# Kernel optimization log

Hardware: AMD Instinct MI355X
Metric: run time of the kernel (lower is better)

## Reference

```python
import jax, jax.numpy as jnp
import numpy as np

B, T, I, H, L, O = 128, 1024, 256, 1024, 2, 128


def setup_inputs() -> dict:
    key = jax.random.key(0)
    ks = jax.random.split(key, 11)
    s = 0.02  # small init scale for stable gates
    inp = {
        "x": jax.random.normal(ks[0], (B, T, I), dtype=jnp.float32),
        # PyTorch LSTM params, gate order (i, f, g, o) stacked along 4H
        "w_ih0": jax.random.normal(ks[1], (4 * H, I), dtype=jnp.float32) * s,
        "w_hh0": jax.random.normal(ks[2], (4 * H, H), dtype=jnp.float32) * s,
        "b_ih0": jax.random.normal(ks[3], (4 * H,), dtype=jnp.float32) * s,
        "b_hh0": jax.random.normal(ks[4], (4 * H,), dtype=jnp.float32) * s,
        "w_ih1": jax.random.normal(ks[5], (4 * H, H), dtype=jnp.float32) * s,
        "w_hh1": jax.random.normal(ks[6], (4 * H, H), dtype=jnp.float32) * s,
        "b_ih1": jax.random.normal(ks[7], (4 * H,), dtype=jnp.float32) * s,
        "b_hh1": jax.random.normal(ks[8], (4 * H,), dtype=jnp.float32) * s,
        "w_out": jax.random.normal(ks[9], (O, H), dtype=jnp.float32) * s,
        "b_out": jax.random.normal(ks[10], (O,), dtype=jnp.float32) * s,
    }
    return inp


def _lstm_layer(x, w_ih, w_hh, b_ih, b_hh):
    # x: [B, T, Din] -> ys: [B, T, H], h_T: [B, H]
    # Precompute input-side gate projections for all timesteps (one big GEMM).
    xg = jnp.einsum("bti,gi->btg", x, w_ih) + b_ih + b_hh  # [B, T, 4H]
    h0 = jnp.zeros((x.shape[0], H), dtype=x.dtype)
    c0 = jnp.zeros((x.shape[0], H), dtype=x.dtype)

    def step(carry, xg_t):
        h, c = carry
        gates = xg_t + h @ w_hh.T  # [B, 4H]
        i, f, g, o = jnp.split(gates, 4, axis=-1)
        i = jax.nn.sigmoid(i)
        f = jax.nn.sigmoid(f)
        g = jnp.tanh(g)
        o = jax.nn.sigmoid(o)
        c_new = f * c + i * g
        h_new = o * jnp.tanh(c_new)
        return (h_new, c_new), h_new

    (h_T, _), ys = jax.lax.scan(step, (h0, c0), jnp.swapaxes(xg, 0, 1))
    return jnp.swapaxes(ys, 0, 1), h_T


def reference(x, w_ih0, w_hh0, b_ih0, b_hh0, w_ih1, w_hh1, b_ih1, b_hh1, w_out, b_out):
    y0, _ = _lstm_layer(x, w_ih0, w_hh0, b_ih0, b_hh0)
    _, h_last = _lstm_layer(y0, w_ih1, w_hh1, b_ih1, b_hh1)
    return h_last @ w_out.T + b_out  # [B, O]
```

## Files before the change

kernel.cpp:

```cpp
#include <hip/hip_runtime.h>
#include <hip/hip_bf16.h>

#define B_ 128
#define T_ 1024
#define I_ 256
#define H_ 1024
#define O_ 128
#define NWG 256
#define HS_ 131072

typedef __attribute__((ext_vector_type(4))) float f32x4;
typedef __attribute__((ext_vector_type(8))) short s16x8;

__device__ __forceinline__ unsigned short f2bf(float f){
  union { float f; unsigned int u; } a; a.f = f;
  unsigned int r = a.u + 0x7FFFu + ((a.u >> 16) & 1u);
  return (unsigned short)(r >> 16);
}
__device__ __forceinline__ float sigmf(float x){ return 1.f/(1.f+__expf(-x)); }
__device__ __forceinline__ float tanhf_(float x){ return 2.f/(1.f+__expf(-2.f*x)) - 1.f; }

__device__ __forceinline__ void ld_frag(s16x8 &d, const unsigned short* p){
  asm volatile("global_load_dwordx4 %0, %1, off sc1" : "=v"(d) : "v"(p) : "memory");
}
__device__ __forceinline__ void ld_f4c(f32x4 &d, const float* p){
  asm volatile("global_load_dwordx4 %0, %1, off sc1" : "=v"(d) : "v"(p) : "memory");
}
__device__ __forceinline__ void st_h(unsigned short* p, unsigned short v){
  __hip_atomic_store(p, v, __ATOMIC_RELAXED, __HIP_MEMORY_SCOPE_AGENT);
}
__device__ __forceinline__ void st_f(float* p, float v){
  __hip_atomic_store(p, v, __ATOMIC_RELAXED, __HIP_MEMORY_SCOPE_AGENT);
}

template<int N>
__device__ __forceinline__ void waitpair(s16x8 &x, s16x8 &y){
  if      constexpr (N==14) asm volatile("s_waitcnt vmcnt(14)" : "+v"(x), "+v"(y) :: "memory");
  else if constexpr (N==12) asm volatile("s_waitcnt vmcnt(12)" : "+v"(x), "+v"(y) :: "memory");
  else if constexpr (N==10) asm volatile("s_waitcnt vmcnt(10)" : "+v"(x), "+v"(y) :: "memory");
  else if constexpr (N==8)  asm volatile("s_waitcnt vmcnt(8)"  : "+v"(x), "+v"(y) :: "memory");
  else if constexpr (N==6)  asm volatile("s_waitcnt vmcnt(6)"  : "+v"(x), "+v"(y) :: "memory");
  else if constexpr (N==4)  asm volatile("s_waitcnt vmcnt(4)"  : "+v"(x), "+v"(y) :: "memory");
  else if constexpr (N==2)  asm volatile("s_waitcnt vmcnt(2)"  : "+v"(x), "+v"(y) :: "memory");
  else                      asm volatile("s_waitcnt vmcnt(0)"  : "+v"(x), "+v"(y) :: "memory");
}
__device__ __forceinline__ void vm_drain(){
  asm volatile("s_waitcnt vmcnt(0)" ::: "memory");
}

__device__ __forceinline__ void bar_arrive(unsigned* base, int gwg, int tid){
  vm_drain();
  __syncthreads();
  if (tid == 0)
    __hip_atomic_fetch_add(&base[(gwg & 7) << 6], 1u, __ATOMIC_RELAXED, __HIP_MEMORY_SCOPE_AGENT);
}
__device__ __forceinline__ void bar_wait(unsigned* base, unsigned tgt32, int tid){
  if (tid < 8){
    while (__hip_atomic_load(&base[tid << 6], __ATOMIC_RELAXED, __HIP_MEMORY_SCOPE_AGENT) < tgt32)
      __builtin_amdgcn_s_sleep(2);
  }
  __syncthreads();
}


__global__ void k_cast_x(const float* __restrict__ x, unsigned short* __restrict__ xb, int n4){
  int i = blockIdx.x*blockDim.x + threadIdx.x;
  if (i >= n4) return;
  f32x4 v = reinterpret_cast<const f32x4*>(x)[i];
  ushort4 o;
  o.x = f2bf(v[0]); o.y = f2bf(v[1]); o.z = f2bf(v[2]); o.w = f2bf(v[3]);
  reinterpret_cast<ushort4*>(xb)[i] = o;
}

__global__ void k_prep_w0(const float* __restrict__ wih, const float* __restrict__ whh,
                          unsigned short* __restrict__ out){
  int n = blockIdx.x*256 + threadIdx.x;
  int j = n & 7, r = (n >> 3) & 15;
  int t = n >> 7;
  int kb = t % 160, gw = t / 160;
  int k = kb*8 + j;
  int grow = (r >> 2)*H_ + gw*4 + (r & 3);
  float v = (k < I_) ? wih[grow*I_ + k] : whh[grow*H_ + (k - I_)];
  out[n] = f2bf(v);
}

__global__ void k_prep_w1(const float* __restrict__ wih, const float* __restrict__ whh,
                          unsigned short* __restrict__ out){
  int n = blockIdx.x*256 + threadIdx.x;
  int j = n & 7, r = (n >> 3) & 15;
  int t = n >> 7;
  int kb = t & 255, gw = t >> 8;
  int k = kb*8 + j;
  int grow = (r >> 2)*H_ + gw*4 + (r & 3);
  float v = (k < H_) ? wih[grow*H_ + k] : whh[grow*H_ + (k - H_)];
  out[n] = f2bf(v);
}

__global__ void k_prep_b(const float* __restrict__ bi0, const float* __restrict__ bh0,
                         const float* __restrict__ bi1, const float* __restrict__ bh1,
                         float* __restrict__ b0, float* __restrict__ b1){
  int n = blockIdx.x*256 + threadIdx.x;
  int layer = n >> 12; int rem = n & 4095;
  int gw = rem >> 4, r = rem & 15;
  int grow = (r >> 2)*H_ + gw*4 + (r & 3);
  if (layer == 0) b0[rem] = bi0[grow] + bh0[grow];
  else            b1[rem] = bi1[grow] + bh1[grow];
}


struct KArgs {
  const unsigned short* xb;
  const float* x32;
  const unsigned short* w0l;
  const unsigned short* w1l;
  const float* b0l;
  const float* b1l;
  unsigned short* h0;
  unsigned short* h1;
  float* hfin;
  const float* wout;
  const float* bout;
  float* y;
  unsigned* cnt;
};

__device__ __forceinline__ void epi(f32x4 (&acc)[2], float (&cs)[2][4], float bias,
                                    unsigned short* __restrict__ hw,
                                    float* __restrict__ hfin,
                                    int wv, int lane, int gwg){
  const int u  = lane & 3;
  const int g0 = (lane >> 2) & 3;
  const int bq = lane >> 4;
  const int ug = (gwg << 2) + u;
  const int kc = ug >> 5;
  const int kg = (ug >> 3) & 3;
  const int jj = ug & 7;
  #pragma unroll
  for (int btl = 0; btl < 2; ++btl){
    const int rb = wv*2 + btl;
    #pragma unroll
    for (int r = 0; r < 4; ++r){
      float pre = acc[btl][r] + bias;
      float q1 = __shfl_xor(pre, 4);
      float q2 = __shfl_xor(pre, 8);
      float q3 = __shfl_xor(pre, 12);
      float iv = (g0==0)?pre:((g0==1)?q1:((g0==2)?q2:q3));
      float fv = (g0==1)?pre:((g0==0)?q1:((g0==3)?q2:q3));
      float gv = (g0==2)?pre:((g0==3)?q1:((g0==0)?q2:q3));
      float ov = (g0==3)?pre:((g0==2)?q1:((g0==1)?q2:q3));
      iv = sigmf(iv); fv = sigmf(fv); gv = tanhf_(gv); ov = sigmf(ov);
      float cn = fv*cs[btl][r] + iv*gv;
      cs[btl][r] = cn;
      float h = ov*tanhf_(cn);
      if (g0 == 0){
        int brow = bq*4 + r;
        int eidx = (((rb*32 + kc) << 9) + (kg*16 + brow)*8 + jj);
        st_h(&hw[eidx], f2bf(h));
        if (hfin) st_f(&hfin[(rb*16 + brow)*H_ + ug], h);
      }
    }
  }
}

#define STEP0(i, NW) { \
  const int s_ = (i) & 7; \
  s16x8 wfn_ = wfc; \
  if ((i) + 1 < 32) wfn_ = *(const s16x8*)(sW0 + ((9 + (i)) << 9) + (lane << 3)); \
  waitpair<NW>(fr[s_][0], fr[s_][1]); \
  acc0[0] = __builtin_amdgcn_mfma_f32_16x16x32_bf16(fr[s_][0], wfc, acc0[0], 0, 0, 0); \
  acc0[1] = __builtin_amdgcn_mfma_f32_16x16x32_bf16(fr[s_][1], wfc, acc0[1], 0, 0, 0); \
  if ((i) + 8 < 32){ \
    ld_frag(fr[s_][0], h0r + ((rdA + (i) + 8) << 9) + l8); \
    ld_frag(fr[s_][1], h0r + ((rdB + (i) + 8) << 9) + l8); } \
  wfc = wfn_; }

#define STEP1(i, NW) { \
  const int s_ = (i) & 7; \
  s16x8 wfn_ = wfc; \
  if ((i) + 1 < 64) wfn_ = *(const s16x8*)(sW1 + (((i) + 1) << 9) + (lane << 3)); \
  waitpair<NW>(fr[s_][0], fr[s_][1]); \
  acc1[0] = __builtin_amdgcn_mfma_f32_16x16x32_bf16(fr[s_][0], wfc, acc1[0], 0, 0, 0); \
  acc1[1] = __builtin_amdgcn_mfma_f32_16x16x32_bf16(fr[s_][1], wfc, acc1[1], 0, 0, 0); \
  if ((i) + 8 < 64){ const int j_ = (i) + 8; \
    const unsigned short* b_ = (j_ < 32) ? h0r : h1r; \
    ld_frag(fr[s_][0], b_ + ((rdA + (j_ & 31)) << 9) + l8); \
    ld_frag(fr[s_][1], b_ + ((rdB + (j_ & 31)) << 9) + l8); } \
  wfc = wfn_; }

__global__ void __launch_bounds__(256, 1) k_lstm(KArgs a){
  extern __shared__ char smem[];
  unsigned short* sW0 = (unsigned short*)smem;
  unsigned short* sW1 = (unsigned short*)(smem + 40960);
  float* sB    = (float*)(smem + 106496);

  const int tid  = threadIdx.x;
  const int gwg  = blockIdx.x;
  const int wv   = tid >> 6;
  const int lane = tid & 63;
  const int lrow = lane & 15;
  const int kgrp = lane >> 4;
  const int koff = kgrp << 3;

  {
    const s16x8* s0 = (const s16x8*)a.w0l + gwg*2560;
    s16x8* d0 = (s16x8*)sW0;
    for (int i = tid; i < 2560; i += 256) d0[i] = s0[i];
    const s16x8* s1 = (const s16x8*)a.w1l + gwg*4096;
    s16x8* d1 = (s16x8*)sW1;
    for (int i = tid; i < 4096; i += 256) d1[i] = s1[i];
    if (tid < 16){ sB[tid] = a.b0l[gwg*16 + tid]; sB[16 + tid] = a.b1l[gwg*16 + tid]; }
  }
  __syncthreads();

  const float bias0 = sB[lrow];
  const float bias1 = sB[16 + lrow];
  float c0s[2][4] = {{0,0,0,0},{0,0,0,0}};
  float c1s[2][4] = {{0,0,0,0},{0,0,0,0}};

  const int rdA = (wv*2 + 0) << 5;
  const int rdB = (wv*2 + 1) << 5;
  const int l8  = lane << 3;
  const size_t xoff0 = (size_t)((wv*2 + 0)*16 + lrow)*(T_*I_) + koff;
  const size_t xoff1 = (size_t)((wv*2 + 1)*16 + lrow)*(T_*I_) + koff;
  const f32x4 z = {0.f, 0.f, 0.f, 0.f};

  int m3 = 0, m3p1 = 1, m3p2 = 2;

  for (int p = 0; p <= T_; ++p){
    const unsigned short* __restrict__ h0r = a.h0 + m3p2*HS_;
    const unsigned short* __restrict__ h1r = a.h1 + m3p1*HS_;
    unsigned short* __restrict__ h0w = a.h0 + m3  *HS_;
    unsigned short* __restrict__ h1w = a.h1 + m3p2*HS_;

    f32x4 acc0[2] = {z, z};
    if (p < T_){
      if (a.xb){
        const unsigned short* xp0 = a.xb + xoff0 + p*I_;
        const unsigned short* xp1 = a.xb + xoff1 + p*I_;
        #pragma unroll
        for (int kc = 0; kc < 8; ++kc){
          s16x8 wf = *(const s16x8*)(sW0 + (kc << 9) + (lane << 3));
          s16x8 a0 = *(const s16x8*)(xp0 + (kc << 5));
          s16x8 a1 = *(const s16x8*)(xp1 + (kc << 5));
          acc0[0] = __builtin_amdgcn_mfma_f32_16x16x32_bf16(a0, wf, acc0[0], 0, 0, 0);
          acc0[1] = __builtin_amdgcn_mfma_f32_16x16x32_bf16(a1, wf, acc0[1], 0, 0, 0);
        }
      } else {
        const float* fx0 = a.x32 + xoff0 + p*I_;
        const float* fx1 = a.x32 + xoff1 + p*I_;
        #pragma unroll
        for (int kc = 0; kc < 8; ++kc){
          s16x8 wf = *(const s16x8*)(sW0 + (kc << 9) + (lane << 3));
          union { s16x8 v; unsigned short us[8]; } t0, t1;
          f32x4 p00 = *(const f32x4*)(fx0 + (kc << 5));
          f32x4 p01 = *(const f32x4*)(fx0 + (kc << 5) + 4);
          f32x4 p10 = *(const f32x4*)(fx1 + (kc << 5));
          f32x4 p11 = *(const f32x4*)(fx1 + (kc << 5) + 4);
          #pragma unroll
          for (int j2 = 0; j2 < 4; ++j2){
            t0.us[j2] = f2bf(p00[j2]); t0.us[4+j2] = f2bf(p01[j2]);
            t1.us[j2] = f2bf(p10[j2]); t1.us[4+j2] = f2bf(p11[j2]);
          }
          acc0[0] = __builtin_amdgcn_mfma_f32_16x16x32_bf16(t0.v, wf, acc0[0], 0, 0, 0);
          acc0[1] = __builtin_amdgcn_mfma_f32_16x16x32_bf16(t1.v, wf, acc0[1], 0, 0, 0);
        }
      }
    }

    if (p > 0) bar_wait(a.cnt, 32u * (unsigned)p, tid);

    if (p < T_){
      vm_drain();
      s16x8 fr[8][2];
      #pragma unroll
      for (int s2 = 0; s2 < 8; ++s2){
        ld_frag(fr[s2][0], h0r + ((rdA + s2) << 9) + l8);
        ld_frag(fr[s2][1], h0r + ((rdB + s2) << 9) + l8);
      }
      s16x8 wfc = *(const s16x8*)(sW0 + (8 << 9) + (lane << 3));
      #pragma unroll
      for (int i = 0; i < 25; ++i) STEP0(i, 14);
      STEP0(25,12); STEP0(26,10); STEP0(27,8); STEP0(28,6);
      STEP0(29,4);  STEP0(30,2);  STEP0(31,0);
      epi(acc0, c0s, bias0, h0w, nullptr, wv, lane, gwg);
    }

    if (p > 0){
      f32x4 acc1[2] = {z, z};
      vm_drain();
      s16x8 fr[8][2];
      #pragma unroll
      for (int s2 = 0; s2 < 8; ++s2){
        ld_frag(fr[s2][0], h0r + ((rdA + s2) << 9) + l8);
        ld_frag(fr[s2][1], h0r + ((rdB + s2) << 9) + l8);
      }
      s16x8 wfc = *(const s16x8*)(sW1 + (lane << 3));
      #pragma unroll
      for (int i = 0; i < 57; ++i) STEP1(i, 14);
      STEP1(57,12); STEP1(58,10); STEP1(59,8); STEP1(60,6);
      STEP1(61,4);  STEP1(62,2);  STEP1(63,0);
      epi(acc1, c1s, bias1, h1w, (p == T_) ? a.hfin : nullptr, wv, lane, gwg);
    }

    bar_arrive(a.cnt, gwg, tid);

    m3 = m3p1; m3p1 = m3p2; m3p2 = (m3p2 == 2) ? 0 : m3p2 + 1;
  }

  bar_wait(a.cnt, 32u * (unsigned)(T_ + 1), tid);

  if (gwg < 64){
    const int b = (gwg >> 3)*16 + (tid >> 4);
    const int o = (gwg & 7)*16 + (tid & 15);
    const float* hb = a.hfin + b*H_;
    const f32x4* wr = (const f32x4*)(a.wout + o*H_);
    float s = a.bout[o];
    for (int g = 0; g < 32; ++g){
      f32x4 t0,t1,t2,t3,t4,t5,t6,t7;
      ld_f4c(t0, hb + g*32 +  0); ld_f4c(t1, hb + g*32 +  4);
      ld_f4c(t2, hb + g*32 +  8); ld_f4c(t3, hb + g*32 + 12);
      ld_f4c(t4, hb + g*32 + 16); ld_f4c(t5, hb + g*32 + 20);
      ld_f4c(t6, hb + g*32 + 24); ld_f4c(t7, hb + g*32 + 28);
      asm volatile("s_waitcnt vmcnt(0)"
        : "+v"(t0),"+v"(t1),"+v"(t2),"+v"(t3),"+v"(t4),"+v"(t5),"+v"(t6),"+v"(t7) :: "memory");
      const f32x4 w0 = wr[g*8+0], w1 = wr[g*8+1], w2 = wr[g*8+2], w3 = wr[g*8+3];
      const f32x4 w4 = wr[g*8+4], w5 = wr[g*8+5], w6 = wr[g*8+6], w7 = wr[g*8+7];
      s += t0[0]*w0[0]+t0[1]*w0[1]+t0[2]*w0[2]+t0[3]*w0[3];
      s += t1[0]*w1[0]+t1[1]*w1[1]+t1[2]*w1[2]+t1[3]*w1[3];
      s += t2[0]*w2[0]+t2[1]*w2[1]+t2[2]*w2[2]+t2[3]*w2[3];
      s += t3[0]*w3[0]+t3[1]*w3[1]+t3[2]*w3[2]+t3[3]*w3[3];
      s += t4[0]*w4[0]+t4[1]*w4[1]+t4[2]*w4[2]+t4[3]*w4[3];
      s += t5[0]*w5[0]+t5[1]*w5[1]+t5[2]*w5[2]+t5[3]*w5[3];
      s += t6[0]*w6[0]+t6[1]*w6[1]+t6[2]*w6[2]+t6[3]*w6[3];
      s += t7[0]*w7[0]+t7[1]*w7[1]+t7[2]*w7[2]+t7[3]*w7[3];
    }
    a.y[b*O_ + o] = s;
  }
}


extern "C" void kernel_launch(void* const* d_in, const int* in_sizes, int n_in,
                              void* d_out, int out_size, void* d_ws, size_t ws_size,
                              hipStream_t stream){
  const float* x    = (const float*)d_in[0];
  const float* wih0 = (const float*)d_in[1];
  const float* whh0 = (const float*)d_in[2];
  const float* bih0 = (const float*)d_in[3];
  const float* bhh0 = (const float*)d_in[4];
  const float* wih1 = (const float*)d_in[5];
  const float* whh1 = (const float*)d_in[6];
  const float* bih1 = (const float*)d_in[7];
  const float* bhh1 = (const float*)d_in[8];
  const float* wout = (const float*)d_in[9];
  const float* bout = (const float*)d_in[10];
  float* y = (float*)d_out;

  char* ws = (char*)d_ws;
  size_t off = 0;
  auto alloc = [&](size_t n){ char* p = ws + off; off += (n + 255) & ~(size_t)255; return p; };

  unsigned* cnt = (unsigned*)alloc(2048);
  unsigned short* w0l = (unsigned short*)alloc((size_t)256*160*16*8*2);
  unsigned short* w1l = (unsigned short*)alloc((size_t)256*256*16*8*2);
  float* b0l  = (float*)alloc(256*16*4);
  float* b1l  = (float*)alloc(256*16*4);
  unsigned short* h0 = (unsigned short*)alloc((size_t)3*HS_*2);
  unsigned short* h1 = (unsigned short*)alloc((size_t)3*HS_*2);
  float* hfin = (float*)alloc((size_t)B_*H_*4);
  unsigned short* xb = nullptr;
  size_t xb_bytes = (size_t)B_*T_*I_*2;
  if (ws_size >= off + xb_bytes + 256) xb = (unsigned short*)alloc(xb_bytes);

  hipMemsetAsync(cnt, 0, 2048, stream);
  hipMemsetAsync(h0, 0, (size_t)3*HS_*2, stream);
  hipMemsetAsync(h1, 0, (size_t)3*HS_*2, stream);

  if (xb) k_cast_x<<<dim3((B_*T_*I_/4 + 255)/256), dim3(256), 0, stream>>>(x, xb, B_*T_*I_/4);
  k_prep_w0<<<dim3(5242880/256), dim3(256), 0, stream>>>(wih0, whh0, w0l);
  k_prep_w1<<<dim3(8388608/256), dim3(256), 0, stream>>>(wih1, whh1, w1l);
  k_prep_b<<<dim3(32), dim3(256), 0, stream>>>(bih0, bhh0, bih1, bhh1, b0l, b1l);

  KArgs args;
  args.xb = xb; args.x32 = x;
  args.w0l = w0l; args.w1l = w1l; args.b0l = b0l; args.b1l = b1l;
  args.h0 = h0; args.h1 = h1; args.hfin = hfin;
  args.wout = wout; args.bout = bout; args.y = y;
  args.cnt = cnt;

  (void)hipFuncSetAttribute((const void*)k_lstm,
                            hipFuncAttributeMaxDynamicSharedMemorySize, 106624);
  void* kp[] = { (void*)&args };
  hipLaunchCooperativeKernel((void*)k_lstm, dim3(NWG), dim3(256), kp, 106624, stream);
}
```

Before: 13.86 ms.

## Share layer-0 hidden-state fragments between both LSTM layers' recurrent GEMMs

Each step previously loaded the layer-0 hidden state from global memory twice: once for layer 0's recurrent GEMM and again for the first half of layer 1's input GEMM. The loops are now fused so each loaded h0 fragment feeds both layer-0 and layer-1 MFMAs, followed by a separate loop over the layer-1 recurrent half. This cuts about a third of the per-step global fragment loads on the serial critical path. The cost is two live accumulator sets and two weight streams, which raises register pressure, plus MFMA work that is discarded at the first and last steps. A fallback to a normal launch is also added in case the cooperative launch fails.

Result: faster. 11.46 ms (median of 2 runs) (-17.3%).

```diff
diff --git a/kernel.cpp b/kernel.cpp
--- a/kernel.cpp
+++ b/kernel.cpp
@@ -162,30 +162,36 @@
   }
 }
 
-#define STEP0(i, NW) { \
+#define MFMA_(A, Bf, C) __builtin_amdgcn_mfma_f32_16x16x32_bf16(A, Bf, C, 0, 0, 0)
+
+#define FUS(i) { \
   const int s_ = (i) & 7; \
-  s16x8 wfn_ = wfc; \
-  if ((i) + 1 < 32) wfn_ = *(const s16x8*)(sW0 + ((9 + (i)) << 9) + (lane << 3)); \
+  s16x8 w0n_ = wfc, w1n_; \
+  if ((i) + 1 < 32) w0n_ = *(const s16x8*)(sW0 + ((9 + (i)) << 9) + (lane << 3)); \
+  w1n_ = *(const s16x8*)(sW1 + (((i) + 1) << 9) + (lane << 3)); \
+  waitpair<14>(fr[s_][0], fr[s_][1]); \
+  acc0[0] = MFMA_(fr[s_][0], wfc, acc0[0]); \
+  acc0[1] = MFMA_(fr[s_][1], wfc, acc0[1]); \
+  acc1[0] = MFMA_(fr[s_][0], wf1c, acc1[0]); \
+  acc1[1] = MFMA_(fr[s_][1], wf1c, acc1[1]); \
+  { const int j_ = (i) + 8; \
+    const unsigned short* b_ = (j_ < 32) ? h0r : h1r; \
+    const int c_ = j_ & 31; \
+    ld_frag(fr[s_][0], b_ + ((rdA + c_) << 9) + l8); \
+    ld_frag(fr[s_][1], b_ + ((rdB + c_) << 9) + l8); } \
+  wfc = w0n_; wf1c = w1n_; }
+
+#define ST2(j, NW) { \
+  const int s_ = (j) & 7; \
+  s16x8 w1n_ = wf1c; \
+  if ((j) + 1 < 32) w1n_ = *(const s16x8*)(sW1 + ((33 + (j)) << 9) + (lane << 3)); \
   waitpair<NW>(fr[s_][0], fr[s_][1]); \
-  acc0[0] = __builtin_amdgcn_mfma_f32_16x16x32_bf16(fr[s_][0], wfc, acc0[0], 0, 0, 0); \
-  acc0[1] = __builtin_amdgcn_mfma_f32_16x16x32_bf16(fr[s_][1], wfc, acc0[1], 0, 0, 0); \
-  if ((i) + 8 < 32){ \
-    ld_frag(fr[s_][0], h0r + ((rdA + (i) + 8) << 9) + l8); \
-    ld_frag(fr[s_][1], h0r + ((rdB + (i) + 8) << 9) + l8); } \
-  wfc = wfn_; }
-
-#define STEP1(i, NW) { \
-  const int s_ = (i) & 7; \
-  s16x8 wfn_ = wfc; \
-  if ((i) + 1 < 64) wfn_ = *(const s16x8*)(sW1 + (((i) + 1) << 9) + (lane << 3)); \
-  waitpair<NW>(fr[s_][0], fr[s_][1]); \
-  acc1[0] = __builtin_amdgcn_mfma_f32_16x16x32_bf16(fr[s_][0], wfc, acc1[0], 0, 0, 0); \
-  acc1[1] = __builtin_amdgcn_mfma_f32_16x16x32_bf16(fr[s_][1], wfc, acc1[1], 0, 0, 0); \
-  if ((i) + 8 < 64){ const int j_ = (i) + 8; \
-    const unsigned short* b_ = (j_ < 32) ? h0r : h1r; \
-    ld_frag(fr[s_][0], b_ + ((rdA + (j_ & 31)) << 9) + l8); \
-    ld_frag(fr[s_][1], b_ + ((rdB + (j_ & 31)) << 9) + l8); } \
-  wfc = wfn_; }
+  acc1[0] = MFMA_(fr[s_][0], wf1c, acc1[0]); \
+  acc1[1] = MFMA_(fr[s_][1], wf1c, acc1[1]); \
+  if ((j) + 8 < 32){ const int c_ = (j) + 8; \
+    ld_frag(fr[s_][0], h1r + ((rdA + c_) << 9) + l8); \
+    ld_frag(fr[s_][1], h1r + ((rdB + c_) << 9) + l8); } \
+  wf1c = w1n_; }
 
 __global__ void __launch_bounds__(256, 1) k_lstm(KArgs a){
   extern __shared__ char smem[];
@@ -233,6 +239,7 @@
     unsigned short* __restrict__ h1w = a.h1 + m3p2*HS_;
 
     f32x4 acc0[2] = {z, z};
+    f32x4 acc1[2] = {z, z};
     if (p < T_){
       if (a.xb){
         const unsigned short* xp0 = a.xb + xoff0 + p*I_;
@@ -242,8 +249,8 @@
           s16x8 wf = *(const s16x8*)(sW0 + (kc << 9) + (lane << 3));
           s16x8 a0 = *(const s16x8*)(xp0 + (kc << 5));
           s16x8 a1 = *(const s16x8*)(xp1 + (kc << 5));
-          acc0[0] = __builtin_amdgcn_mfma_f32_16x16x32_bf16(a0, wf, acc0[0], 0, 0, 0);
-          acc0[1] = __builtin_amdgcn_mfma_f32_16x16x32_bf16(a1, wf, acc0[1], 0, 0, 0);
+          acc0[0] = MFMA_(a0, wf, acc0[0]);
+          acc0[1] = MFMA_(a1, wf, acc0[1]);
         }
       } else {
         const float* fx0 = a.x32 + xoff0 + p*I_;
@@ -261,45 +268,32 @@
             t0.us[j2] = f2bf(p00[j2]); t0.us[4+j2] = f2bf(p01[j2]);
             t1.us[j2] = f2bf(p10[j2]); t1.us[4+j2] = f2bf(p11[j2]);
           }
-          acc0[0] = __builtin_amdgcn_mfma_f32_16x16x32_bf16(t0.v, wf, acc0[0], 0, 0, 0);
-          acc0[1] = __builtin_amdgcn_mfma_f32_16x16x32_bf16(t1.v, wf, acc0[1], 0, 0, 0);
+          acc0[0] = MFMA_(t0.v, wf, acc0[0]);
+          acc0[1] = MFMA_(t1.v, wf, acc0[1]);
         }
       }
     }
 
     if (p > 0) bar_wait(a.cnt, 32u * (unsigned)p, tid);
 
-    if (p < T_){
-      vm_drain();
+    vm_drain();
+    {
       s16x8 fr[8][2];
       #pragma unroll
       for (int s2 = 0; s2 < 8; ++s2){
         ld_frag(fr[s2][0], h0r + ((rdA + s2) << 9) + l8);
         ld_frag(fr[s2][1], h0r + ((rdB + s2) << 9) + l8);
       }
-      s16x8 wfc = *(const s16x8*)(sW0 + (8 << 9) + (lane << 3));
+      s16x8 wfc  = *(const s16x8*)(sW0 + (8 << 9) + (lane << 3));
+      s16x8 wf1c = *(const s16x8*)(sW1 + (lane << 3));
       #pragma unroll
-      for (int i = 0; i < 25; ++i) STEP0(i, 14);
-      STEP0(25,12); STEP0(26,10); STEP0(27,8); STEP0(28,6);
-      STEP0(29,4);  STEP0(30,2);  STEP0(31,0);
-      epi(acc0, c0s, bias0, h0w, nullptr, wv, lane, gwg);
-    }
-
-    if (p > 0){
-      f32x4 acc1[2] = {z, z};
-      vm_drain();
-      s16x8 fr[8][2];
+      for (int i = 0; i < 32; ++i) FUS(i);
+      if (p < T_) epi(acc0, c0s, bias0, h0w, nullptr, wv, lane, gwg);
       #pragma unroll
-      for (int s2 = 0; s2 < 8; ++s2){
-        ld_frag(fr[s2][0], h0r + ((rdA + s2) << 9) + l8);
-        ld_frag(fr[s2][1], h0r + ((rdB + s2) << 9) + l8);
-      }
-      s16x8 wfc = *(const s16x8*)(sW1 + (lane << 3));
-      #pragma unroll
-      for (int i = 0; i < 57; ++i) STEP1(i, 14);
-      STEP1(57,12); STEP1(58,10); STEP1(59,8); STEP1(60,6);
-      STEP1(61,4);  STEP1(62,2);  STEP1(63,0);
-      epi(acc1, c1s, bias1, h1w, (p == T_) ? a.hfin : nullptr, wv, lane, gwg);
+      for (int j = 0; j < 24; ++j) ST2(j, 14);
+      ST2(24,14); ST2(25,12); ST2(26,10); ST2(27,8);
+      ST2(28,6);  ST2(29,4);  ST2(30,2);  ST2(31,0);
+      if (p > 0) epi(acc1, c1s, bias1, h1w, (p == T_) ? a.hfin : nullptr, wv, lane, gwg);
     }
 
     bar_arrive(a.cnt, gwg, tid);
@@ -390,5 +384,9 @@
   (void)hipFuncSetAttribute((const void*)k_lstm,
                             hipFuncAttributeMaxDynamicSharedMemorySize, 106624);
   void* kp[] = { (void*)&args };
-  hipLaunchCooperativeKernel((void*)k_lstm, dim3(NWG), dim3(256), kp, 106624, stream);
-}
+  hipError_t e = hipLaunchCooperativeKernel((void*)k_lstm, dim3(NWG), dim3(256),
+                                            kp, 106624, stream);
+  if (e != hipSuccess){
+    k_lstm<<<dim3(NWG), dim3(256), 106624, stream>>>(args);
+  }
+}
```

## Split workgroups by layer, double per-WG tile, and use per-wave barriers with packed stores

Applied to the files above, without the earlier changes.

Workgroups are now dedicated to one layer each: 128 run layer 0 and 128 run layer 1. Each handles two hidden-unit tiles, so it issues four MFMAs per h-fragment load instead of two, halving redundant h reads per unit of work. The epilogue gathers bf16 h values with lane shuffles into 16-byte vector stores in place of scalar atomic stores. The grid barrier now arrives and waits per wave rather than per block, dropping __syncthreads from the step loop. The trade-offs are more LDS per workgroup (131 KB) and more barrier atomics per step, and the removed block-level sync could expose ordering hazards between waves.

Measured after the change: 21.06 ms. 52.0% more time.

```diff
diff --git a/kernel.cpp b/kernel.cpp
--- a/kernel.cpp
+++ b/kernel.cpp
@@ -11,6 +11,7 @@
 
 typedef __attribute__((ext_vector_type(4))) float f32x4;
 typedef __attribute__((ext_vector_type(8))) short s16x8;
+typedef __attribute__((ext_vector_type(4))) unsigned u32x4;
 
 __device__ __forceinline__ unsigned short f2bf(float f){
   union { float f; unsigned int u; } a; a.f = f;
@@ -26,8 +27,8 @@
 __device__ __forceinline__ void ld_f4c(f32x4 &d, const float* p){
   asm volatile("global_load_dwordx4 %0, %1, off sc1" : "=v"(d) : "v"(p) : "memory");
 }
-__device__ __forceinline__ void st_h(unsigned short* p, unsigned short v){
-  __hip_atomic_store(p, v, __ATOMIC_RELAXED, __HIP_MEMORY_SCOPE_AGENT);
+__device__ __forceinline__ void st16(unsigned short* p, u32x4 v){
+  asm volatile("global_store_dwordx4 %0, %1, off sc1" :: "v"(p), "v"(v) : "memory");
 }
 __device__ __forceinline__ void st_f(float* p, float v){
   __hip_atomic_store(p, v, __ATOMIC_RELAXED, __HIP_MEMORY_SCOPE_AGENT);
@@ -48,18 +49,16 @@
   asm volatile("s_waitcnt vmcnt(0)" ::: "memory");
 }
 
-__device__ __forceinline__ void bar_arrive(unsigned* base, int gwg, int tid){
+__device__ __forceinline__ void wbar_arrive(unsigned* base, int gwg, int lane){
   vm_drain();
-  __syncthreads();
-  if (tid == 0)
+  if (lane == 0)
     __hip_atomic_fetch_add(&base[(gwg & 7) << 6], 1u, __ATOMIC_RELAXED, __HIP_MEMORY_SCOPE_AGENT);
 }
-__device__ __forceinline__ void bar_wait(unsigned* base, unsigned tgt32, int tid){
-  if (tid < 8){
-    while (__hip_atomic_load(&base[tid << 6], __ATOMIC_RELAXED, __HIP_MEMORY_SCOPE_AGENT) < tgt32)
+__device__ __forceinline__ void wbar_wait(unsigned* base, unsigned tgt, int lane){
+  if (lane < 8){
+    while (__hip_atomic_load(&base[lane << 6], __ATOMIC_RELAXED, __HIP_MEMORY_SCOPE_AGENT) < tgt)
       __builtin_amdgcn_s_sleep(2);
   }
-  __syncthreads();
 }
 
 
@@ -124,77 +123,128 @@
   unsigned* cnt;
 };
 
-__device__ __forceinline__ void epi(f32x4 (&acc)[2], float (&cs)[2][4], float bias,
-                                    unsigned short* __restrict__ hw,
-                                    float* __restrict__ hfin,
-                                    int wv, int lane, int gwg){
+__device__ __forceinline__ void epiPack(f32x4 (&accL)[2], f32x4 (&accH)[2],
+                                        float (&csL)[2][4], float (&csH)[2][4],
+                                        float biasL, float biasH,
+                                        unsigned short* __restrict__ hw,
+                                        float* __restrict__ hfin,
+                                        int wv, int lane, int w){
   const int u  = lane & 3;
   const int g0 = (lane >> 2) & 3;
   const int bq = lane >> 4;
-  const int ug = (gwg << 2) + u;
-  const int kc = ug >> 5;
-  const int kg = (ug >> 3) & 3;
-  const int jj = ug & 7;
+  const int kc = w >> 2;
+  const int kg = w & 3;
   #pragma unroll
   for (int btl = 0; btl < 2; ++btl){
     const int rb = wv*2 + btl;
+    unsigned bL[4], bH[4];
     #pragma unroll
     for (int r = 0; r < 4; ++r){
-      float pre = acc[btl][r] + bias;
-      float q1 = __shfl_xor(pre, 4);
-      float q2 = __shfl_xor(pre, 8);
-      float q3 = __shfl_xor(pre, 12);
-      float iv = (g0==0)?pre:((g0==1)?q1:((g0==2)?q2:q3));
-      float fv = (g0==1)?pre:((g0==0)?q1:((g0==3)?q2:q3));
-      float gv = (g0==2)?pre:((g0==3)?q1:((g0==0)?q2:q3));
-      float ov = (g0==3)?pre:((g0==2)?q1:((g0==1)?q2:q3));
+      float preL = accL[btl][r] + biasL;
+      float q1 = __shfl_xor(preL, 4);
+      float q2 = __shfl_xor(preL, 8);
+      float q3 = __shfl_xor(preL, 12);
+      float iv = (g0==0)?preL:((g0==1)?q1:((g0==2)?q2:q3));
+      float fv = (g0==1)?preL:((g0==0)?q1:((g0==3)?q2:q3));
+      float gv = (g0==2)?preL:((g0==3)?q1:((g0==0)?q2:q3));
+      float ov = (g0==3)?preL:((g0==2)?q1:((g0==1)?q2:q3));
       iv = sigmf(iv); fv = sigmf(fv); gv = tanhf_(gv); ov = sigmf(ov);
-      float cn = fv*cs[btl][r] + iv*gv;
-      cs[btl][r] = cn;
-      float h = ov*tanhf_(cn);
-      if (g0 == 0){
+      float cnL = fv*csL[btl][r] + iv*gv;
+      csL[btl][r] = cnL;
+      float hL = ov*tanhf_(cnL);
+      float preH = accH[btl][r] + biasH;
+      q1 = __shfl_xor(preH, 4);
+      q2 = __shfl_xor(preH, 8);
+      q3 = __shfl_xor(preH, 12);
+      iv = (g0==0)?preH:((g0==1)?q1:((g0==2)?q2:q3));
+      fv = (g0==1)?preH:((g0==0)?q1:((g0==3)?q2:q3));
+      gv = (g0==2)?preH:((g0==3)?q1:((g0==0)?q2:q3));
+      ov = (g0==3)?preH:((g0==2)?q1:((g0==1)?q2:q3));
+      iv = sigmf(iv); fv = sigmf(fv); gv = tanhf_(gv); ov = sigmf(ov);
+      float cnH = fv*csH[btl][r] + iv*gv;
+      csH[btl][r] = cnH;
+      float hH = ov*tanhf_(cnH);
+      bL[r] = (unsigned)f2bf(hL);
+      bH[r] = (unsigned)f2bf(hH);
+      if (hfin && g0 == 0){
         int brow = bq*4 + r;
-        int eidx = (((rb*32 + kc) << 9) + (kg*16 + brow)*8 + jj);
-        st_h(&hw[eidx], f2bf(h));
-        if (hfin) st_f(&hfin[(rb*16 + brow)*H_ + ug], h);
+        st_f(&hfin[(rb*16 + brow)*H_ + 8*w + u], hL);
+        st_f(&hfin[(rb*16 + brow)*H_ + 8*w + 4 + u], hH);
       }
     }
-  }
-}
-
-#define STEP0(i, NW) { \
+    unsigned sh[4];
+    #pragma unroll
+    for (int r = 0; r < 4; ++r) sh[r] = (unsigned)__shfl_xor((int)bL[r^1], 1);
+    #pragma unroll
+    for (int r = 0; r < 4; ++r) bL[r] = ((u^r)&1) ? sh[r] : bL[r];
+    #pragma unroll
+    for (int r = 0; r < 4; ++r) sh[r] = (unsigned)__shfl_xor((int)bL[r^2], 2);
+    #pragma unroll
+    for (int r = 0; r < 4; ++r) bL[r] = ((u^r)&2) ? sh[r] : bL[r];
+    #pragma unroll
+    for (int r = 0; r < 4; ++r) sh[r] = (unsigned)__shfl_xor((int)bH[r^1], 1);
+    #pragma unroll
+    for (int r = 0; r < 4; ++r) bH[r] = ((u^r)&1) ? sh[r] : bH[r];
+    #pragma unroll
+    for (int r = 0; r < 4; ++r) sh[r] = (unsigned)__shfl_xor((int)bH[r^2], 2);
+    #pragma unroll
+    for (int r = 0; r < 4; ++r) bH[r] = ((u^r)&2) ? sh[r] : bH[r];
+    if (g0 == 0){
+      u32x4 val;
+      val[0] = bL[0] | (bL[1] << 16);
+      val[1] = bL[2] | (bL[3] << 16);
+      val[2] = bH[0] | (bH[1] << 16);
+      val[3] = bH[2] | (bH[3] << 16);
+      unsigned short* p = hw + (((rb*32 + kc) << 9) + (kg*16 + bq*4 + u)*8);
+      st16(p, val);
+    }
+  }
+}
+
+#define MFMA_(A, Bf, C) __builtin_amdgcn_mfma_f32_16x16x32_bf16(A, Bf, C, 0, 0, 0)
+
+#define L0S(i, NW) { \
   const int s_ = (i) & 7; \
-  s16x8 wfn_ = wfc; \
-  if ((i) + 1 < 32) wfn_ = *(const s16x8*)(sW0 + ((9 + (i)) << 9) + (lane << 3)); \
+  s16x8 wLn_ = wfLc, wHn_ = wfHc; \
+  if ((i) + 1 < 32){ \
+    wLn_ = *(const s16x8*)(sW + ((9 + (i)) << 9) + l8w); \
+    wHn_ = *(const s16x8*)(sW + 20480 + ((9 + (i)) << 9) + l8w); } \
   waitpair<NW>(fr[s_][0], fr[s_][1]); \
-  acc0[0] = __builtin_amdgcn_mfma_f32_16x16x32_bf16(fr[s_][0], wfc, acc0[0], 0, 0, 0); \
-  acc0[1] = __builtin_amdgcn_mfma_f32_16x16x32_bf16(fr[s_][1], wfc, acc0[1], 0, 0, 0); \
+  accL[0] = MFMA_(fr[s_][0], wfLc, accL[0]); \
+  accL[1] = MFMA_(fr[s_][1], wfLc, accL[1]); \
+  accH[0] = MFMA_(fr[s_][0], wfHc, accH[0]); \
+  accH[1] = MFMA_(fr[s_][1], wfHc, accH[1]); \
   if ((i) + 8 < 32){ \
     ld_frag(fr[s_][0], h0r + ((rdA + (i) + 8) << 9) + l8); \
     ld_frag(fr[s_][1], h0r + ((rdB + (i) + 8) << 9) + l8); } \
-  wfc = wfn_; }
-
-#define STEP1(i, NW) { \
+  wfLc = wLn_; wfHc = wHn_; }
+
+#define L1S(i, NW) { \
   const int s_ = (i) & 7; \
-  s16x8 wfn_ = wfc; \
-  if ((i) + 1 < 64) wfn_ = *(const s16x8*)(sW1 + (((i) + 1) << 9) + (lane << 3)); \
+  s16x8 wLn_ = wfLc, wHn_ = wfHc; \
+  if ((i) + 1 < 64){ \
+    wLn_ = *(const s16x8*)(sW + (((i) + 1) << 9) + l8w); \
+    wHn_ = *(const s16x8*)(sW + 32768 + (((i) + 1) << 9) + l8w); } \
   waitpair<NW>(fr[s_][0], fr[s_][1]); \
-  acc1[0] = __builtin_amdgcn_mfma_f32_16x16x32_bf16(fr[s_][0], wfc, acc1[0], 0, 0, 0); \
-  acc1[1] = __builtin_amdgcn_mfma_f32_16x16x32_bf16(fr[s_][1], wfc, acc1[1], 0, 0, 0); \
+  accL[0] = MFMA_(fr[s_][0], wfLc, accL[0]); \
+  accL[1] = MFMA_(fr[s_][1], wfLc, accL[1]); \
+  accH[0] = MFMA_(fr[s_][0], wfHc, accH[0]); \
+  accH[1] = MFMA_(fr[s_][1], wfHc, accH[1]); \
   if ((i) + 8 < 64){ const int j_ = (i) + 8; \
     const unsigned short* b_ = (j_ < 32) ? h0r : h1r; \
     ld_frag(fr[s_][0], b_ + ((rdA + (j_ & 31)) << 9) + l8); \
     ld_frag(fr[s_][1], b_ + ((rdB + (j_ & 31)) << 9) + l8); } \
-  wfc = wfn_; }
+  wfLc = wLn_; wfHc = wHn_; }
 
 __global__ void __launch_bounds__(256, 1) k_lstm(KArgs a){
   extern __shared__ char smem[];
-  unsigned short* sW0 = (unsigned short*)smem;
-  unsigned short* sW1 = (unsigned short*)(smem + 40960);
-  float* sB    = (float*)(smem + 106496);
+  unsigned short* sW = (unsigned short*)smem;
+  float* sB = (float*)(smem + 131072);
 
   const int tid  = threadIdx.x;
   const int gwg  = blockIdx.x;
+  const bool isL1 = gwg >= 128;
+  const int w    = gwg & 127;
   const int wv   = tid >> 6;
   const int lane = tid & 63;
   const int lrow = lane & 15;
@@ -202,24 +252,29 @@
   const int koff = kgrp << 3;
 
   {
-    const s16x8* s0 = (const s16x8*)a.w0l + gwg*2560;
-    s16x8* d0 = (s16x8*)sW0;
-    for (int i = tid; i < 2560; i += 256) d0[i] = s0[i];
-    const s16x8* s1 = (const s16x8*)a.w1l + gwg*4096;
-    s16x8* d1 = (s16x8*)sW1;
-    for (int i = tid; i < 4096; i += 256) d1[i] = s1[i];
-    if (tid < 16){ sB[tid] = a.b0l[gwg*16 + tid]; sB[16 + tid] = a.b1l[gwg*16 + tid]; }
+    if (isL1){
+      const s16x8* s1 = (const s16x8*)a.w1l + (size_t)(2*w)*4096;
+      s16x8* d = (s16x8*)sW;
+      for (int i = tid; i < 8192; i += 256) d[i] = s1[i];
+      if (tid < 32) sB[tid] = a.b1l[w*32 + tid];
+    } else {
+      const s16x8* s0 = (const s16x8*)a.w0l + (size_t)(2*w)*2560;
+      s16x8* d = (s16x8*)sW;
+      for (int i = tid; i < 5120; i += 256) d[i] = s0[i];
+      if (tid < 32) sB[tid] = a.b0l[w*32 + tid];
+    }
   }
   __syncthreads();
 
-  const float bias0 = sB[lrow];
-  const float bias1 = sB[16 + lrow];
-  float c0s[2][4] = {{0,0,0,0},{0,0,0,0}};
-  float c1s[2][4] = {{0,0,0,0},{0,0,0,0}};
+  const float biasL = sB[lrow];
+  const float biasH = sB[16 + lrow];
+  float csL[2][4] = {{0,0,0,0},{0,0,0,0}};
+  float csH[2][4] = {{0,0,0,0},{0,0,0,0}};
 
   const int rdA = (wv*2 + 0) << 5;
   const int rdB = (wv*2 + 1) << 5;
   const int l8  = lane << 3;
+  const int l8w = lane << 3;
   const size_t xoff0 = (size_t)((wv*2 + 0)*16 + lrow)*(T_*I_) + koff;
   const size_t xoff1 = (size_t)((wv*2 + 1)*16 + lrow)*(T_*I_) + koff;
   const f32x4 z = {0.f, 0.f, 0.f, 0.f};
@@ -232,82 +287,94 @@
     unsigned short* __restrict__ h0w = a.h0 + m3  *HS_;
     unsigned short* __restrict__ h1w = a.h1 + m3p2*HS_;
 
-    f32x4 acc0[2] = {z, z};
-    if (p < T_){
+    f32x4 accL[2] = {z, z};
+    f32x4 accH[2] = {z, z};
+
+    if (!isL1 && p < T_){
       if (a.xb){
-        const unsigned short* xp0 = a.xb + xoff0 + p*I_;
-        const unsigned short* xp1 = a.xb + xoff1 + p*I_;
-        #pragma unroll
-        for (int kc = 0; kc < 8; ++kc){
-          s16x8 wf = *(const s16x8*)(sW0 + (kc << 9) + (lane << 3));
-          s16x8 a0 = *(const s16x8*)(xp0 + (kc << 5));
-          s16x8 a1 = *(const s16x8*)(xp1 + (kc << 5));
-          acc0[0] = __builtin_amdgcn_mfma_f32_16x16x32_bf16(a0, wf, acc0[0], 0, 0, 0);
-          acc0[1] = __builtin_amdgcn_mfma_f32_16x16x32_bf16(a1, wf, acc0[1], 0, 0, 0);
+        const unsigned short* xp0 = a.xb + xoff0 + (size_t)p*I_;
+        const unsigned short* xp1 = a.xb + xoff1 + (size_t)p*I_;
+        #pragma unroll
+        for (int kc2 = 0; kc2 < 8; ++kc2){
+          s16x8 wfL = *(const s16x8*)(sW + (kc2 << 9) + l8w);
+          s16x8 wfH = *(const s16x8*)(sW + 20480 + (kc2 << 9) + l8w);
+          s16x8 a0 = *(const s16x8*)(xp0 + (kc2 << 5));
+          s16x8 a1 = *(const s16x8*)(xp1 + (kc2 << 5));
+          accL[0] = MFMA_(a0, wfL, accL[0]);
+          accL[1] = MFMA_(a1, wfL, accL[1]);
+          accH[0] = MFMA_(a0, wfH, accH[0]);
+          accH[1] = MFMA_(a1, wfH, accH[1]);
         }
       } else {
-        const float* fx0 = a.x32 + xoff0 + p*I_;
-        const float* fx1 = a.x32 + xoff1 + p*I_;
-        #pragma unroll
-        for (int kc = 0; kc < 8; ++kc){
-          s16x8 wf = *(const s16x8*)(sW0 + (kc << 9) + (lane << 3));
+        const float* fx0 = a.x32 + xoff0 + (size_t)p*I_;
+        const float* fx1 = a.x32 + xoff1 + (size_t)p*I_;
+        #pragma unroll
+        for (int kc2 = 0; kc2 < 8; ++kc2){
+          s16x8 wfL = *(const s16x8*)(sW + (kc2 << 9) + l8w);
+          s16x8 wfH = *(const s16x8*)(sW + 20480 + (kc2 << 9) + l8w);
           union { s16x8 v; unsigned short us[8]; } t0, t1;
-          f32x4 p00 = *(const f32x4*)(fx0 + (kc << 5));
-          f32x4 p01 = *(const f32x4*)(fx0 + (kc << 5) + 4);
-          f32x4 p10 = *(const f32x4*)(fx1 + (kc << 5));
-          f32x4 p11 = *(const f32x4*)(fx1 + (kc << 5) + 4);
+          f32x4 p00 = *(const f32x4*)(fx0 + (kc2 << 5));
+          f32x4 p01 = *(const f32x4*)(fx0 + (kc2 << 5) + 4);
+          f32x4 p10 = *(const f32x4*)(fx1 + (kc2 << 5));
+          f32x4 p11 = *(const f32x4*)(fx1 + (kc2 << 5) + 4);
           #pragma unroll
           for (int j2 = 0; j2 < 4; ++j2){
             t0.us[j2] = f2bf(p00[j2]); t0.us[4+j2] = f2bf(p01[j2]);
             t1.us[j2] = f2bf(p10[j2]); t1.us[4+j2] = f2bf(p11[j2]);
           }
-          acc0[0] = __builtin_amdgcn_mfma_f32_16x16x32_bf16(t0.v, wf, acc0[0], 0, 0, 0);
-          acc0[1] = __builtin_amdgcn_mfma_f32_16x16x32_bf16(t1.v, wf, acc0[1], 0, 0, 0);
+          accL[0] = MFMA_(t0.v, wfL, accL[0]);
+          accL[1] = MFMA_(t1.v, wfL, accL[1]);
+          accH[0] = MFMA_(t0.v, wfH, accH[0]);
+          accH[1] = MFMA_(t1.v, wfH, accH[1]);
         }
       }
     }
 
-    if (p > 0) bar_wait(a.cnt, 32u * (unsigned)p, tid);
-
-    if (p < T_){
-      vm_drain();
-      s16x8 fr[8][2];
-      #pragma unroll
-      for (int s2 = 0; s2 < 8; ++s2){
-        ld_frag(fr[s2][0], h0r + ((rdA + s2) << 9) + l8);
-        ld_frag(fr[s2][1], h0r + ((rdB + s2) << 9) + l8);
+    if (p > 0) wbar_wait(a.cnt, 128u * (unsigned)p, lane);
+
+    if (!isL1){
+      if (p < T_){
+        vm_drain();
+        s16x8 fr[8][2];
+        #pragma unroll
+        for (int s2 = 0; s2 < 8; ++s2){
+          ld_frag(fr[s2][0], h0r + ((rdA + s2) << 9) + l8);
+          ld_frag(fr[s2][1], h0r + ((rdB + s2) << 9) + l8);
+        }
+        s16x8 wfLc = *(const s16x8*)(sW + (8 << 9) + l8w);
+        s16x8 wfHc = *(const s16x8*)(sW + 20480 + (8 << 9) + l8w);
+        #pragma unroll
+        for (int i = 0; i < 25; ++i) L0S(i, 14);
+        L0S(25,12); L0S(26,10); L0S(27,8); L0S(28,6);
+        L0S(29,4);  L0S(30,2);  L0S(31,0);
+        epiPack(accL, accH, csL, csH, biasL, biasH, h0w, nullptr, wv, lane, w);
       }
-      s16x8 wfc = *(const s16x8*)(sW0 + (8 << 9) + (lane << 3));
-      #pragma unroll
-      for (int i = 0; i < 25; ++i) STEP0(i, 14);
-      STEP0(25,12); STEP0(26,10); STEP0(27,8); STEP0(28,6);
-      STEP0(29,4);  STEP0(30,2);  STEP0(31,0);
-      epi(acc0, c0s, bias0, h0w, nullptr, wv, lane, gwg);
-    }
-
-    if (p > 0){
-      f32x4 acc1[2] = {z, z};
-      vm_drain();
-      s16x8 fr[8][2];
-      #pragma unroll
-      for (int s2 = 0; s2 < 8; ++s2){
-        ld_frag(fr[s2][0], h0r + ((rdA + s2) << 9) + l8);
-        ld_frag(fr[s2][1], h0r + ((rdB + s2) << 9) + l8);
+    } else {
+      if (p > 0){
+        vm_drain();
+        s16x8 fr[8][2];
+        #pragma unroll
+        for (int s2 = 0; s2 < 8; ++s2){
+          ld_frag(fr[s2][0], h0r + ((rdA + s2) << 9) + l8);
+          ld_frag(fr[s2][1], h0r + ((rdB + s2) << 9) + l8);
+        }
+        s16x8 wfLc = *(const s16x8*)(sW + l8w);
+        s16x8 wfHc = *(const s16x8*)(sW + 32768 + l8w);
+        #pragma unroll
+        for (int i = 0; i < 57; ++i) L1S(i, 14);
+        L1S(57,12); L1S(58,10); L1S(59,8); L1S(60,6);
+        L1S(61,4);  L1S(62,2);  L1S(63,0);
+        epiPack(accL, accH, csL, csH, biasL, biasH, h1w,
+                (p == T_) ? a.hfin : nullptr, wv, lane, w);
       }
-      s16x8 wfc = *(const s16x8*)(sW1 + (lane << 3));
-      #pragma unroll
-      for (int i = 0; i < 57; ++i) STEP1(i, 14);
-      STEP1(57,12); STEP1(58,10); STEP1(59,8); STEP1(60,6);
-      STEP1(61,4);  STEP1(62,2);  STEP1(63,0);
-      epi(acc1, c1s, bias1, h1w, (p == T_) ? a.hfin : nullptr, wv, lane, gwg);
-    }
-
-    bar_arrive(a.cnt, gwg, tid);
+    }
+
+    wbar_arrive(a.cnt, gwg, lane);
 
     m3 = m3p1; m3p1 = m3p2; m3p2 = (m3p2 == 2) ? 0 : m3p2 + 1;
   }
 
-  bar_wait(a.cnt, 32u * (unsigned)(T_ + 1), tid);
+  wbar_wait(a.cnt, 128u * (unsigned)(T_ + 1), lane);
 
   if (gwg < 64){
     const int b = (gwg >> 3)*16 + (tid >> 4);
@@ -388,7 +455,11 @@
   args.cnt = cnt;
 
   (void)hipFuncSetAttribute((const void*)k_lstm,
-                            hipFuncAttributeMaxDynamicSharedMemorySize, 106624);
+                            hipFuncAttributeMaxDynamicSharedMemorySize, 131200);
   void* kp[] = { (void*)&args };
-  hipLaunchCooperativeKernel((void*)k_lstm, dim3(NWG), dim3(256), kp, 106624, stream);
-}
+  hipError_t e = hipLaunchCooperativeKernel((void*)k_lstm, dim3(NWG), dim3(256),
+                                            kp, 131200, stream);
+  if (e != hipSuccess){
+    k_lstm<<<dim3(NWG), dim3(256), 131200, stream>>>(args);
+  }
+}
```
